# Kernel tuning notes

Measured on AMD Instinct MI355X. Metric: run time of the kernel, lower is better.

The kernel has to match this reference:

```python
import jax, jax.numpy as jnp
import numpy as np

TOP_K = 50  # init default top_k=50
EPS = 1e-12  # torch F.normalize eps


def setup_inputs() -> dict:
    key = jax.random.key(0)
    k1, k2, k3, k4 = jax.random.split(key, 4)
    d = 128
    P = 2048      # number of test patches
    M = 100000    # memory bank size
    return {
        "test_patches": jax.random.normal(k1, (P, d), jnp.float32),
        "memory_nodes": jax.random.normal(k2, (M, d), jnp.float32),
        "W1": jax.random.normal(k3, (d, d // 2), jnp.float32) * 0.05,
        "b1": jnp.zeros((d // 2,), jnp.float32),
        "W2": jax.random.normal(k4, (d // 2, 1), jnp.float32) * 0.05,
        "b2": jnp.zeros((1,), jnp.float32),
    }


def reference(test_patches, memory_nodes, W1, b1, W2, b2):
    P = test_patches.shape[0]
    M = memory_nodes.shape[0]
    K = min(TOP_K, M)

    # --- compute_exact_topk_edges ---
    sim = test_patches @ memory_nodes.T              # [P, M] dense similarity
    _, topk_idx = jax.lax.top_k(sim, K)              # [P, K], sorted descending like torch.topk
    test_idx = jnp.broadcast_to(jnp.arange(P, dtype=topk_idx.dtype)[:, None], (P, K)).reshape(-1)
    edge_index = jnp.stack([topk_idx.reshape(-1), test_idx], axis=0)  # [2, P*K] (memory_idx, test_idx)

    # --- token_evidence_pooling (on test_patches) ---
    logits = jax.nn.relu(test_patches @ W1 + b1) @ W2 + b2  # [P, 1]
    weights = jax.nn.softmax(logits, axis=0)                 # softmax over patches
    g = jnp.sum(test_patches * weights, axis=0, keepdims=True)  # [1, d]
    g = g / jnp.maximum(jnp.linalg.norm(g, axis=-1, keepdims=True), EPS)
    return edge_index, g
```

## Files before the change

kernel.cpp:

```cpp
#include <hip/hip_runtime.h>
#include <math.h>

#define D    128
#define PN   2048
#define MN   100000
#define KK   50
#define NEGF (-3.0e38f)
#define NCB  782
#define NRB  16
#define NCP  128
#define SCAP 16
#define PB_CVTB 6256
#define PB_CVTA (PB_CVTB + 128)
#define PB_TAU  (PB_CVTA + 512)
#define PB_ALL  (PB_TAU + 512)

typedef __attribute__((ext_vector_type(8))) short short8;
typedef __attribute__((ext_vector_type(4))) float f32x4;

__device__ __forceinline__ bool pgtf(float va, int ia, float vb, int ib) {
  return (va > vb) || (va == vb && ia < ib);
}

__device__ __forceinline__ unsigned short f2bf(float x) {
  union { float f; unsigned u; } c; c.f = x;
  unsigned r = c.u + 0x7FFFu + ((c.u >> 16) & 1u);
  return (unsigned short)(r >> 16);
}

__device__ __forceinline__ void gload_lds16(const void* g, void* l) {
  __builtin_amdgcn_global_load_lds((const __attribute__((address_space(1))) void*)g,
                                   (__attribute__((address_space(3))) void*)l, 16, 0, 0);
}

__global__ __launch_bounds__(256)
void k_prep(const float* __restrict__ X, const float* __restrict__ Bn,
            const float* __restrict__ W1, const float* __restrict__ b1,
            const float* __restrict__ W2, const float* __restrict__ b2,
            short* __restrict__ Ap, short* __restrict__ Bp,
            float* __restrict__ tau, float* __restrict__ logits) {
  const int b   = blockIdx.x;
  const int tid = threadIdx.x;

  if (b < PB_CVTB) {
    int q = b * 256 + tid;
    int cb = q >> 11, t = q & 2047;
    int ct = t >> 8, ks = (t >> 6) & 3, l = t & 63;
    int n  = cb * 128 + ct * 16 + (l & 15);
    int k0 = ks * 32 + (l >> 4) * 8;
    short8 h = {0, 0, 0, 0, 0, 0, 0, 0};
    if (n < MN) {
      const float4* s = (const float4*)(Bn + (size_t)n * D + k0);
      float4 f0 = s[0], f1 = s[1];
      h[0]=(short)f2bf(f0.x); h[1]=(short)f2bf(f0.y); h[2]=(short)f2bf(f0.z); h[3]=(short)f2bf(f0.w);
      h[4]=(short)f2bf(f1.x); h[5]=(short)f2bf(f1.y); h[6]=(short)f2bf(f1.z); h[7]=(short)f2bf(f1.w);
    }
    *(short8*)(Bp + (size_t)q * 8) = h;
  } else if (b < PB_CVTA) {
    int q = (b - PB_CVTB) * 256 + tid;
    int rb = q >> 11, t = q & 2047;
    int rt = t >> 8, ks = (t >> 6) & 3, l = t & 63;
    int m  = rb * 128 + rt * 16 + (l & 15);
    int k0 = ks * 32 + (l >> 4) * 8;
    const float4* s = (const float4*)(X + (size_t)m * D + k0);
    float4 f0 = s[0], f1 = s[1];
    short8 h;
    h[0]=(short)f2bf(f0.x); h[1]=(short)f2bf(f0.y); h[2]=(short)f2bf(f0.z); h[3]=(short)f2bf(f0.w);
    h[4]=(short)f2bf(f1.x); h[5]=(short)f2bf(f1.y); h[6]=(short)f2bf(f1.z); h[7]=(short)f2bf(f1.w);
    *(short8*)(Ap + (size_t)q * 8) = h;
  } else if (b < PB_TAU) {
    int w = tid >> 6, lane = tid & 63;
    int row = (b - PB_CVTA) * 4 + w;
    float v0 = X[(size_t)row * D + lane];
    float v1 = X[(size_t)row * D + 64 + lane];
    float s = v0 * v0 + v1 * v1;
#pragma unroll
    for (int st = 32; st > 0; st >>= 1) s += __shfl_xor(s, st, 64);
    if (lane == 0) tau[row] = 3.0f * sqrtf(s);
  } else {
    int w = tid >> 6, lane = tid & 63;
    int p = (b - PB_TAU) * 4 + w;
    const float* xp = X + (size_t)p * D;
    double h = (double)b1[lane];
#pragma unroll 4
    for (int k = 0; k < D; ++k) h += (double)xp[k] * (double)W1[k * 64 + lane];
    float hf = fmaxf((float)h, 0.f);
    double y = (double)hf * (double)W2[lane];
#pragma unroll
    for (int s = 32; s > 0; s >>= 1) y += __shfl_xor(y, s, 64);
    if (lane == 0) logits[p] = (float)(y + (double)b2[0]);
  }
}

__global__ __launch_bounds__(256, 2)
void k_sim_cand(const short* __restrict__ Ap, const short* __restrict__ Bp,
                const float* __restrict__ tau,
                unsigned short* __restrict__ cand2, unsigned char* __restrict__ cnt2) {
  __shared__ short Bs[2][2048 * 8];
  __shared__ float tauL[128];
  __shared__ int   lcnt[128];
  __shared__ unsigned short lcand[128][SCAP];

  const int tid  = threadIdx.x;
  const int lane = tid & 63;
  const int wq   = __builtin_amdgcn_readfirstlane(tid >> 6);
  const int rb   = blockIdx.x >> 7;
  const int cp   = blockIdx.x & 127;
  const int row0 = rb * 128;

  if (tid < 128) { tauL[tid] = tau[row0 + tid]; lcnt[tid] = 0; }

  const int rtb = (wq >> 1) * 4;
  const int ctb = (wq & 1) * 4;

  short8 a[4][4];
  const short8* gA = (const short8*)(Ap + (size_t)rb * (2048 * 8));
#pragma unroll
  for (int rt = 0; rt < 4; ++rt)
#pragma unroll
    for (int ks = 0; ks < 4; ++ks)
      a[rt][ks] = gA[((rtb + rt) * 4 + ks) * 64 + lane];

  {
    const char* g = (const char*)Bp + (size_t)cp * 32768;
#pragma unroll
    for (int j = 0; j < 8; ++j)
      gload_lds16(g + (wq * 8 + j) * 1024 + lane * 16, (char*)&Bs[0][0] + (wq * 8 + j) * 1024);
  }
  __syncthreads();

  const int colb = ctb * 16 + (lane & 15);
  const int rql  = (lane >> 4) * 4;

  int c = cp, buf = 0;

#pragma unroll 1
  for (int i = 0; ; ++i) {
    int cn = cp + (i + 1) * NCP;
    if (cn < NCB) {
      const char* g = (const char*)Bp + (size_t)cn * 32768;
#pragma unroll
      for (int j = 0; j < 8; ++j)
        gload_lds16(g + (wq * 8 + j) * 1024 + lane * 16,
                    (char*)&Bs[buf ^ 1][0] + (wq * 8 + j) * 1024);
    }

    const short8* lB = (const short8*)&Bs[buf][0];
    f32x4 acc[4][4] = {};
#pragma unroll
    for (int ks = 0; ks < 4; ++ks) {
      short8 b[4];
#pragma unroll
      for (int ct = 0; ct < 4; ++ct) b[ct] = lB[((ctb + ct) * 4 + ks) * 64 + lane];
#pragma unroll
      for (int rt = 0; rt < 4; ++rt)
#pragma unroll
        for (int ct = 0; ct < 4; ++ct)
          acc[rt][ct] = __builtin_amdgcn_mfma_f32_16x16x32_bf16(a[rt][ks], b[ct], acc[rt][ct], 0, 0, 0);
    }

    unsigned m0 = 0, m1 = 0;
#pragma unroll
    for (int rt = 0; rt < 4; ++rt) {
#pragma unroll
      for (int rg = 0; rg < 4; ++rg) {
        float t = tauL[(rtb + rt) * 16 + rql + rg];
#pragma unroll
        for (int ct = 0; ct < 4; ++ct) {
          unsigned bit = (unsigned)(rt * 16 + rg * 4 + ct);
          unsigned h = (acc[rt][ct][rg] >= t) ? 1u : 0u;
          if (rt < 2) m0 |= h << bit;
          else        m1 |= h << (bit - 32);
        }
      }
    }
    int cbase = c * 128;
#pragma unroll 1
    while (m0 | m1) {
      int s;
      if (m0) { s = __builtin_ctz(m0); m0 &= m0 - 1; }
      else    { s = 32 + __builtin_ctz(m1); m1 &= m1 - 1; }
      int rt = s >> 4, rg = (s >> 2) & 3, ct = s & 3;
      int col_l = colb + ct * 16;
      if (cbase + col_l < MN) {
        int row_l = (rtb + rt) * 16 + rql + rg;
        int pos = atomicAdd(&lcnt[row_l], 1);
        if (pos < SCAP) lcand[row_l][pos] = (unsigned short)((i << 7) | col_l);
      }
    }

    if (cn >= NCB) break;
    c = cn; buf ^= 1;
    __syncthreads();
  }

  __syncthreads();
  if (tid < 128) {
    int cc = lcnt[tid]; if (cc > SCAP) cc = SCAP;
    size_t strip = (size_t)(row0 + tid) * NCP + cp;
    cnt2[strip] = (unsigned char)cc;
#pragma unroll 1
    for (int q = 0; q < cc; ++q) cand2[strip * SCAP + q] = lcand[tid][q];
  }
}

__global__ __launch_bounds__(512)
void k_select(const unsigned short* __restrict__ cand2, const unsigned char* __restrict__ cnt2,
              const float* __restrict__ A, const float* __restrict__ Bn,
              float* __restrict__ out) {
  __shared__ float Ash[D];
  __shared__ int   ixsh[512];
  __shared__ float svsh[512];
  __shared__ int   nsh;

  const int row  = blockIdx.x;
  const int tid  = threadIdx.x;
  const int lane = tid & 63;

  if (tid < D / 4) ((float4*)Ash)[tid] = ((const float4*)(A + (size_t)row * D))[tid];

  if (tid < 64) {
    size_t s0 = (size_t)row * NCP + lane;
    size_t s1 = s0 + 64;
    int c0 = cnt2[s0], c1 = cnt2[s1];
    int x = c0 + c1, incl = x;
#pragma unroll
    for (int d2 = 1; d2 < 64; d2 <<= 1) {
      int y = __shfl_up(incl, d2, 64);
      if (lane >= d2) incl += y;
    }
    int off = incl - x;
    int n = __shfl(incl, 63, 64);
    if (n > 512) n = 512;
#pragma unroll 1
    for (int q = 0; q < c0; ++q) {
      int code = cand2[s0 * SCAP + q];
      int pos = off + q;
      if (pos < 512) ixsh[pos] = lane * 128 + (code >> 7) * (NCP * 128) + (code & 127);
    }
#pragma unroll 1
    for (int q = 0; q < c1; ++q) {
      int code = cand2[s1 * SCAP + q];
      int pos = off + c0 + q;
      if (pos < 512) ixsh[pos] = (lane + 64) * 128 + (code >> 7) * (NCP * 128) + (code & 127);
    }
    if (lane == 0) nsh = n;
  }
  __syncthreads();
  const int n = nsh;

  if (tid < n) {
    int gc = ixsh[tid];
    const float4* Br = (const float4*)(Bn + (size_t)gc * D);
    float ae = 0.f, ao = 0.f;
#pragma unroll 1
    for (int kb = 0; kb < 8; ++kb) {
      float4 b0 = Br[kb * 4 + 0];
      float4 b1 = Br[kb * 4 + 1];
      float4 b2 = Br[kb * 4 + 2];
      float4 b3 = Br[kb * 4 + 3];
      const float* Ak = Ash + kb * 16;
      ae = __builtin_fmaf(Ak[0],  b0.x, ae); ao = __builtin_fmaf(Ak[1],  b0.y, ao);
      ae = __builtin_fmaf(Ak[2],  b0.z, ae); ao = __builtin_fmaf(Ak[3],  b0.w, ao);
      ae = __builtin_fmaf(Ak[4],  b1.x, ae); ao = __builtin_fmaf(Ak[5],  b1.y, ao);
      ae = __builtin_fmaf(Ak[6],  b1.z, ae); ao = __builtin_fmaf(Ak[7],  b1.w, ao);
      ae = __builtin_fmaf(Ak[8],  b2.x, ae); ao = __builtin_fmaf(Ak[9],  b2.y, ao);
      ae = __builtin_fmaf(Ak[10], b2.z, ae); ao = __builtin_fmaf(Ak[11], b2.w, ao);
      ae = __builtin_fmaf(Ak[12], b3.x, ae); ao = __builtin_fmaf(Ak[13], b3.y, ao);
      ae = __builtin_fmaf(Ak[14], b3.z, ae); ao = __builtin_fmaf(Ak[15], b3.w, ao);
    }
    svsh[tid] = ae + ao;
  } else {
    svsh[tid] = NEGF;
    ixsh[tid] = 0x40000000 + tid;
  }
  __syncthreads();

#pragma unroll 1
  for (int size = 2; size <= 512; size <<= 1) {
#pragma unroll 1
    for (int stride = size >> 1; stride > 0; stride >>= 1) {
      if (tid < 256) {
        int l = ((tid & ~(stride - 1)) << 1) | (tid & (stride - 1));
        int m = l | stride;
        bool desc = ((l & size) == 0);
        float vl = svsh[l], vm = svsh[m];
        int   il = ixsh[l], im = ixsh[m];
        bool g = pgtf(vm, im, vl, il);
        if (g == desc) {
          svsh[l] = vm; svsh[m] = vl;
          ixsh[l] = im; ixsh[m] = il;
        }
      }
      __syncthreads();
    }
  }

  if (tid < KK) {
    out[(size_t)row * KK + tid] = (float)ixsh[tid];
    out[(size_t)(PN * KK) + (size_t)row * KK + tid] = (float)row;
  }
}

__global__ __launch_bounds__(1024)
void k_pool(const float* __restrict__ X, const float* __restrict__ logits,
            float* __restrict__ outg) {
  __shared__ float  wsum[2048];
  __shared__ double red[1024];
  __shared__ double part[1024];
  int t = threadIdx.x;
  float a = logits[t], b = logits[t + 1024];
  red[t] = (double)fmaxf(a, b);
  __syncthreads();
  for (int s = 512; s > 0; s >>= 1) { if (t < s) red[t] = fmax(red[t], red[t + s]); __syncthreads(); }
  float m = (float)red[0];
  __syncthreads();
  float e0 = expf(a - m), e1 = expf(b - m);
  wsum[t] = e0; wsum[t + 1024] = e1;
  red[t] = (double)e0 + (double)e1;
  __syncthreads();
  for (int s = 512; s > 0; s >>= 1) { if (t < s) red[t] += red[t + s]; __syncthreads(); }
  double S = red[0];
  __syncthreads();
  int dim = t & 127, q = t >> 7;
  const float* xq = X + (size_t)(q * 256) * D + dim;
  double accd = 0.0;
#pragma unroll 4
  for (int p = 0; p < 256; ++p) accd += (double)wsum[q * 256 + p] * (double)xq[(size_t)p * D];
  part[t] = accd;
  __syncthreads();
  double gval = 0.0;
  if (t < 128) {
    double g = 0.0;
#pragma unroll
    for (int q2 = 0; q2 < 8; ++q2) g += part[q2 * 128 + t];
    g /= S;
    gval = g;
    red[t] = g * g;
  }
  __syncthreads();
  for (int s = 64; s > 0; s >>= 1) { if (t < s) red[t] += red[t + s]; __syncthreads(); }
  if (t < 128) {
    double nrm = sqrt(red[0]);
    outg[t] = (float)(gval / fmax(nrm, 1e-12));
  }
}

extern "C" void kernel_launch(void* const* d_in, const int* in_sizes, int n_in,
                              void* d_out, int out_size, void* d_ws, size_t ws_size,
                              hipStream_t stream) {
  const float* X  = (const float*)d_in[0];
  const float* Bn = (const float*)d_in[1];
  const float* W1 = (const float*)d_in[2];
  const float* b1 = (const float*)d_in[3];
  const float* W2 = (const float*)d_in[4];
  const float* b2 = (const float*)d_in[5];
  float* out = (float*)d_out;

  char* p = (char*)d_ws;
  unsigned short* cand2 = (unsigned short*)p; p += (size_t)PN * NCP * SCAP * 2;
  unsigned char*  cnt2  = (unsigned char*)p;  p += (size_t)PN * NCP;
  float* tau    = (float*)p;                  p += (size_t)PN * 4;
  float* logits = (float*)p;                  p += (size_t)PN * 4;
  short* Ap     = (short*)p;                  p += (size_t)NRB * 2048 * 8 * 2;
  short* Bp     = (short*)p;

  k_prep<<<PB_ALL, 256, 0, stream>>>(X, Bn, W1, b1, W2, b2, Ap, Bp, tau, logits);
  k_pool<<<1, 1024, 0, stream>>>(X, logits, out + (size_t)2 * PN * KK);
  k_sim_cand<<<NRB * NCP, 256, 0, stream>>>(Ap, Bp, tau, cand2, cnt2);
  k_select<<<PN, 512, 0, stream>>>(cand2, cnt2, X, Bn, out);
}
```

Baseline: 230.8 us.

## Fuse pooling into select kernel, hoist tau loads, simplify candidate emission

Removes the separate single-block pooling kernel launch by running the softmax pooling as an extra block 0 of the select kernel. The candidate-threshold loop in the similarity kernel now keeps tau values in registers and uses a per-row max-of-four early test with direct atomic emission, replacing the bitmask-and-ctz loop. The select dot-product loop is unrolled by two. The main costs targeted are launch overhead and the per-tile threshold test. In exchange, every select block now reserves about 14 KB of extra shared memory, which can lower occupancy, and the unrolled candidate path raises register use.

```diff
diff --git a/kernel.cpp b/kernel.cpp
--- a/kernel.cpp
+++ b/kernel.cpp
@@ -132,6 +132,13 @@
   const int colb = ctb * 16 + (lane & 15);
   const int rql  = (lane >> 4) * 4;
 
+  float tv[4][4];
+#pragma unroll
+  for (int rt = 0; rt < 4; ++rt)
+#pragma unroll
+    for (int rg = 0; rg < 4; ++rg)
+      tv[rt][rg] = tauL[(rtb + rt) * 16 + rql + rg];
+
   int c = cp, buf = 0;
 
 #pragma unroll 1
@@ -159,33 +166,27 @@
           acc[rt][ct] = __builtin_amdgcn_mfma_f32_16x16x32_bf16(a[rt][ks], b[ct], acc[rt][ct], 0, 0, 0);
     }
 
-    unsigned m0 = 0, m1 = 0;
+    int cbase = c * 128;
 #pragma unroll
     for (int rt = 0; rt < 4; ++rt) {
 #pragma unroll
       for (int rg = 0; rg < 4; ++rg) {
-        float t = tauL[(rtb + rt) * 16 + rql + rg];
-#pragma unroll
-        for (int ct = 0; ct < 4; ++ct) {
-          unsigned bit = (unsigned)(rt * 16 + rg * 4 + ct);
-          unsigned h = (acc[rt][ct][rg] >= t) ? 1u : 0u;
-          if (rt < 2) m0 |= h << bit;
-          else        m1 |= h << (bit - 32);
+        float t = tv[rt][rg];
+        float m4 = fmaxf(fmaxf(acc[rt][0][rg], acc[rt][1][rg]),
+                         fmaxf(acc[rt][2][rg], acc[rt][3][rg]));
+        if (m4 >= t) {
+          int row_l = (rtb + rt) * 16 + rql + rg;
+#pragma unroll
+          for (int ct = 0; ct < 4; ++ct) {
+            if (acc[rt][ct][rg] >= t) {
+              int col_l = colb + ct * 16;
+              if (cbase + col_l < MN) {
+                int pos = atomicAdd(&lcnt[row_l], 1);
+                if (pos < SCAP) lcand[row_l][pos] = (unsigned short)((i << 7) | col_l);
+              }
+            }
+          }
         }
-      }
-    }
-    int cbase = c * 128;
-#pragma unroll 1
-    while (m0 | m1) {
-      int s;
-      if (m0) { s = __builtin_ctz(m0); m0 &= m0 - 1; }
-      else    { s = 32 + __builtin_ctz(m1); m1 &= m1 - 1; }
-      int rt = s >> 4, rg = (s >> 2) & 3, ct = s & 3;
-      int col_l = colb + ct * 16;
-      if (cbase + col_l < MN) {
-        int row_l = (rtb + rt) * 16 + rql + rg;
-        int pos = atomicAdd(&lcnt[row_l], 1);
-        if (pos < SCAP) lcand[row_l][pos] = (unsigned short)((i << 7) | col_l);
       }
     }
 
@@ -207,15 +208,62 @@
 __global__ __launch_bounds__(512)
 void k_select(const unsigned short* __restrict__ cand2, const unsigned char* __restrict__ cnt2,
               const float* __restrict__ A, const float* __restrict__ Bn,
-              float* __restrict__ out) {
+              const float* __restrict__ logits, float* __restrict__ out) {
   __shared__ float Ash[D];
   __shared__ int   ixsh[512];
   __shared__ float svsh[512];
   __shared__ int   nsh;
-
-  const int row  = blockIdx.x;
+  __shared__ float  wsum2[2048];
+  __shared__ double redp[512];
+  __shared__ double gpart[128];
+
   const int tid  = threadIdx.x;
   const int lane = tid & 63;
+
+  if (blockIdx.x == 0) {
+    float lv[4];
+    float mx = NEGF;
+#pragma unroll
+    for (int j = 0; j < 4; ++j) { lv[j] = logits[j * 512 + tid]; mx = fmaxf(mx, lv[j]); }
+    redp[tid] = (double)mx;
+    __syncthreads();
+    for (int s = 256; s > 0; s >>= 1) { if (tid < s) redp[tid] = fmax(redp[tid], redp[tid + s]); __syncthreads(); }
+    float m = (float)redp[0];
+    __syncthreads();
+    double ssum = 0.0;
+#pragma unroll
+    for (int j = 0; j < 4; ++j) {
+      float e = expf(lv[j] - m);
+      wsum2[j * 512 + tid] = e;
+      ssum += (double)e;
+    }
+    redp[tid] = ssum;
+    __syncthreads();
+    for (int s = 256; s > 0; s >>= 1) { if (tid < s) redp[tid] += redp[tid + s]; __syncthreads(); }
+    double S = redp[0];
+    __syncthreads();
+    int dim = tid & 127, q = tid >> 7;
+    const float* xq = A + (size_t)(q * 512) * D + dim;
+    double acc = 0.0;
+#pragma unroll 4
+    for (int p = 0; p < 512; ++p) acc += (double)wsum2[q * 512 + p] * (double)xq[(size_t)p * D];
+    redp[tid] = acc;
+    __syncthreads();
+    if (tid < 128) {
+      double g = (redp[tid] + redp[tid + 128] + redp[tid + 256] + redp[tid + 384]) / S;
+      gpart[tid] = g;
+      redp[tid] = g * g;
+    }
+    __syncthreads();
+    for (int s = 64; s > 0; s >>= 1) { if (tid < s) redp[tid] += redp[tid + s]; __syncthreads(); }
+    if (tid < 128) {
+      double nrm = sqrt(redp[0]);
+      out[(size_t)2 * PN * KK + tid] = (float)(gpart[tid] / fmax(nrm, 1e-12));
+    }
+    return;
+  }
+
+  const int row = blockIdx.x - 1;
 
   if (tid < D / 4) ((float4*)Ash)[tid] = ((const float4*)(A + (size_t)row * D))[tid];
 
@@ -253,7 +301,7 @@
     int gc = ixsh[tid];
     const float4* Br = (const float4*)(Bn + (size_t)gc * D);
     float ae = 0.f, ao = 0.f;
-#pragma unroll 1
+#pragma unroll 2
     for (int kb = 0; kb < 8; ++kb) {
       float4 b0 = Br[kb * 4 + 0];
       float4 b1 = Br[kb * 4 + 1];
@@ -302,50 +350,6 @@
   }
 }
 
-__global__ __launch_bounds__(1024)
-void k_pool(const float* __restrict__ X, const float* __restrict__ logits,
-            float* __restrict__ outg) {
-  __shared__ float  wsum[2048];
-  __shared__ double red[1024];
-  __shared__ double part[1024];
-  int t = threadIdx.x;
-  float a = logits[t], b = logits[t + 1024];
-  red[t] = (double)fmaxf(a, b);
-  __syncthreads();
-  for (int s = 512; s > 0; s >>= 1) { if (t < s) red[t] = fmax(red[t], red[t + s]); __syncthreads(); }
-  float m = (float)red[0];
-  __syncthreads();
-  float e0 = expf(a - m), e1 = expf(b - m);
-  wsum[t] = e0; wsum[t + 1024] = e1;
-  red[t] = (double)e0 + (double)e1;
-  __syncthreads();
-  for (int s = 512; s > 0; s >>= 1) { if (t < s) red[t] += red[t + s]; __syncthreads(); }
-  double S = red[0];
-  __syncthreads();
-  int dim = t & 127, q = t >> 7;
-  const float* xq = X + (size_t)(q * 256) * D + dim;
-  double accd = 0.0;
-#pragma unroll 4
-  for (int p = 0; p < 256; ++p) accd += (double)wsum[q * 256 + p] * (double)xq[(size_t)p * D];
-  part[t] = accd;
-  __syncthreads();
-  double gval = 0.0;
-  if (t < 128) {
-    double g = 0.0;
-#pragma unroll
-    for (int q2 = 0; q2 < 8; ++q2) g += part[q2 * 128 + t];
-    g /= S;
-    gval = g;
-    red[t] = g * g;
-  }
-  __syncthreads();
-  for (int s = 64; s > 0; s >>= 1) { if (t < s) red[t] += red[t + s]; __syncthreads(); }
-  if (t < 128) {
-    double nrm = sqrt(red[0]);
-    outg[t] = (float)(gval / fmax(nrm, 1e-12));
-  }
-}
-
 extern "C" void kernel_launch(void* const* d_in, const int* in_sizes, int n_in,
                               void* d_out, int out_size, void* d_ws, size_t ws_size,
                               hipStream_t stream) {
@@ -366,7 +370,6 @@
   short* Bp     = (short*)p;
 
   k_prep<<<PB_ALL, 256, 0, stream>>>(X, Bn, W1, b1, W2, b2, Ap, Bp, tau, logits);
-  k_pool<<<1, 1024, 0, stream>>>(X, logits, out + (size_t)2 * PN * KK);
   k_sim_cand<<<NRB * NCP, 256, 0, stream>>>(Ap, Bp, tau, cand2, cnt2);
-  k_select<<<PN, 512, 0, stream>>>(cand2, cnt2, X, Bn, out);
-}
+  k_select<<<PN + 1, 512, 0, stream>>>(cand2, cnt2, X, Bn, logits, out);
+}
```

Result: slower. 236.6 us (+2.5%).
